# Optimization experiments

Measured on AMD Instinct MI355X. Metric: run time of the kernel, lower is better.

Reference implementation:

```python
import jax, jax.numpy as jnp
import numpy as np

N0, N1, B = 260000, 10240, 1024
E0, E1 = 256000, 10240
IN_C, HID, OUT_C = 602, 256, 41


def setup_inputs() -> dict:
    key = jax.random.key(0)
    ks = jax.random.split(key, 12)
    x = jax.random.normal(ks[0], (N0, IN_C), dtype=jnp.float32)
    W_l0 = jax.random.normal(ks[1], (IN_C, HID), dtype=jnp.float32) / np.sqrt(IN_C)
    b_l0 = jnp.zeros((HID,), dtype=jnp.float32)
    W_r0 = jax.random.normal(ks[2], (IN_C, HID), dtype=jnp.float32) / np.sqrt(IN_C)
    W_l1 = jax.random.normal(ks[3], (HID, OUT_C), dtype=jnp.float32) / np.sqrt(HID)
    b_l1 = jnp.zeros((OUT_C,), dtype=jnp.float32)
    W_r1 = jax.random.normal(ks[4], (HID, OUT_C), dtype=jnp.float32) / np.sqrt(HID)
    src0 = jax.random.randint(ks[5], (E0,), 0, N0)
    dst0 = jnp.sort(jax.random.randint(ks[6], (E0,), 0, N1))
    src1 = jax.random.randint(ks[7], (E1,), 0, N1)
    dst1 = jnp.sort(jax.random.randint(ks[8], (E1,), 0, B))
    return {"x": x, "W_l0": W_l0, "b_l0": b_l0, "W_r0": W_r0,
            "W_l1": W_l1, "b_l1": b_l1, "W_r1": W_r1,
            "src0": src0, "dst0": dst0, "src1": src1, "dst1": dst1}


def _sage_conv(x_src, x_tgt, src, dst, num_tgt, W_l, b_l, W_r):
    # mean aggregation of neighbor messages (PyG SAGEConv, mean aggr)
    msg = x_src[src]                                             # [E, C]
    s = jax.ops.segment_sum(msg, dst, num_segments=num_tgt)     # [Nt, C]
    cnt = jax.ops.segment_sum(jnp.ones((src.shape[0], 1), x_src.dtype),
                              dst, num_segments=num_tgt)         # [Nt, 1]
    agg = s / jnp.maximum(cnt, 1.0)
    # out = lin_l(agg) + lin_r(x_target); lin_r has no bias in PyG
    return agg @ W_l + b_l + x_tgt @ W_r


def reference(x, W_l0, b_l0, W_r0, W_l1, b_l1, W_r1, src0, dst0, src1, dst1):
    # layer 0: N0 sources -> N1 targets (targets are first N1 rows of x)
    h = _sage_conv(x, x[:N1], src0, dst0, N1, W_l0, b_l0, W_r0)
    h = jax.nn.relu(h)  # dropout is identity in eval mode
    # layer 1: N1 sources -> B targets
    out = _sage_conv(h, h[:B], src1, dst1, B, W_l1, b_l1, W_r1)
    return jax.nn.log_softmax(out, axis=-1)
```

## Files before the change

kernel.cpp:

```cpp
#include <hip/hip_runtime.h>
#include <math.h>

constexpr int cN0  = 260000;
constexpr int cN1  = 10240;
constexpr int cB   = 1024;
constexpr int cE0  = 256000;
constexpr int cE1  = 10240;
constexpr int cIN  = 602;
constexpr int cHID = 256;
constexpr int cOUT = 41;
constexpr int KP   = 608;

__device__ __forceinline__ int lower_bound_dev(const int* __restrict__ a, int n, int v) {
    int l = 0, r = n;
    while (l < r) { int m = (l + r) >> 1; if (a[m] < v) l = m + 1; else r = m; }
    return l;
}

__global__ __launch_bounds__(256) void k_agg0(
    const float* __restrict__ x, const int* __restrict__ src0,
    const int* __restrict__ dst0, float* __restrict__ agg0,
    float* __restrict__ xpad)
{
    const int t   = blockIdx.x;
    const int tid = threadIdx.x;
    const int lo  = lower_bound_dev(dst0, cE0, t);
    const int hi  = lower_bound_dev(dst0, cE0, t + 1);
    const int cnt = hi - lo;

    float a0 = 0.f, a1 = 0.f, a2 = 0.f;
    __shared__ int s_src[256];
    for (int base = lo; base < hi; base += 256) {
        const int n = min(256, hi - base);
        __syncthreads();
        if (tid < n) s_src[tid] = src0[base + tid];
        __syncthreads();
        for (int j = 0; j < n; ++j) {
            const float* row = x + (long)s_src[j] * cIN;
            a0 += row[tid];
            a1 += row[tid + 256];
            if (tid < cIN - 512) a2 += row[tid + 512];
        }
    }

    const float inv = 1.f / (float)(cnt > 1 ? cnt : 1);
    float*       og = agg0 + (long)t * KP;
    float*       ox = xpad + (long)t * KP;
    const float* xr = x    + (long)t * cIN;

    og[tid]       = a0 * inv;   ox[tid]       = xr[tid];
    og[tid + 256] = a1 * inv;   ox[tid + 256] = xr[tid + 256];
    if (tid < cIN - 512) {
        og[tid + 512] = a2 * inv;
        ox[tid + 512] = xr[tid + 512];
    } else if (tid < KP - 512) {
        og[tid + 512] = 0.f;
        ox[tid + 512] = 0.f;
    }
}

__global__ __launch_bounds__(256) void k_gemm1(
    const float* __restrict__ agg0, const float* __restrict__ xpad,
    const float* __restrict__ Wl,   const float* __restrict__ Wr,
    const float* __restrict__ bias, float* __restrict__ h)
{
    const int tid = threadIdx.x;
    const int n0  = (blockIdx.x & 3) * 64;
    const int m0  = (blockIdx.x >> 2) * 64;

    __shared__ float As[16][68];
    __shared__ float Bs[16][68];

    float acc[4][4] = {};
    const int tx = tid & 15, ty = tid >> 4;
    const int ai = tid >> 2, ak = (tid & 3) * 4;
    const int bk = tid >> 4, bj = (tid & 15) * 4;

    for (int phase = 0; phase < 2; ++phase) {
        const float* A = phase ? xpad : agg0;
        const float* W = phase ? Wr   : Wl;
        for (int k0 = 0; k0 < KP; k0 += 16) {
            __syncthreads();
            const float4 av = *(const float4*)(A + (long)(m0 + ai) * KP + k0 + ak);
            As[ak + 0][ai] = av.x;
            As[ak + 1][ai] = av.y;
            As[ak + 2][ai] = av.z;
            As[ak + 3][ai] = av.w;
            const int kg = k0 + bk;
            float4 bv = make_float4(0.f, 0.f, 0.f, 0.f);
            if (kg < cIN) bv = *(const float4*)(W + (long)kg * cHID + n0 + bj);
            Bs[bk][bj + 0] = bv.x;
            Bs[bk][bj + 1] = bv.y;
            Bs[bk][bj + 2] = bv.z;
            Bs[bk][bj + 3] = bv.w;
            __syncthreads();
            #pragma unroll
            for (int kk = 0; kk < 16; ++kk) {
                const float4 a4 = *(const float4*)&As[kk][ty * 4];
                const float4 b4 = *(const float4*)&Bs[kk][tx * 4];
                acc[0][0] += a4.x * b4.x; acc[0][1] += a4.x * b4.y;
                acc[0][2] += a4.x * b4.z; acc[0][3] += a4.x * b4.w;
                acc[1][0] += a4.y * b4.x; acc[1][1] += a4.y * b4.y;
                acc[1][2] += a4.y * b4.z; acc[1][3] += a4.y * b4.w;
                acc[2][0] += a4.z * b4.x; acc[2][1] += a4.z * b4.y;
                acc[2][2] += a4.z * b4.z; acc[2][3] += a4.z * b4.w;
                acc[3][0] += a4.w * b4.x; acc[3][1] += a4.w * b4.y;
                acc[3][2] += a4.w * b4.z; acc[3][3] += a4.w * b4.w;
            }
        }
    }

    #pragma unroll
    for (int i = 0; i < 4; ++i) {
        const int m = m0 + ty * 4 + i;
        float4 o;
        o.x = fmaxf(acc[i][0] + bias[n0 + tx * 4 + 0], 0.f);
        o.y = fmaxf(acc[i][1] + bias[n0 + tx * 4 + 1], 0.f);
        o.z = fmaxf(acc[i][2] + bias[n0 + tx * 4 + 2], 0.f);
        o.w = fmaxf(acc[i][3] + bias[n0 + tx * 4 + 3], 0.f);
        *(float4*)(h + (long)m * cHID + n0 + tx * 4) = o;
    }
}

__global__ __launch_bounds__(256) void k_agg1(
    const float* __restrict__ h, const int* __restrict__ src1,
    const int* __restrict__ dst1, float* __restrict__ agg1)
{
    const int t   = blockIdx.x;
    const int tid = threadIdx.x;
    const int lo  = lower_bound_dev(dst1, cE1, t);
    const int hi  = lower_bound_dev(dst1, cE1, t + 1);
    const int cnt = hi - lo;

    float a = 0.f;
    __shared__ int s_src[256];
    for (int base = lo; base < hi; base += 256) {
        const int n = min(256, hi - base);
        __syncthreads();
        if (tid < n) s_src[tid] = src1[base + tid];
        __syncthreads();
        for (int j = 0; j < n; ++j) a += h[(long)s_src[j] * cHID + tid];
    }
    agg1[(long)t * cHID + tid] = a / (float)(cnt > 1 ? cnt : 1);
}

__global__ __launch_bounds__(64) void k_out(
    const float* __restrict__ h,  const float* __restrict__ agg1,
    const float* __restrict__ Wl, const float* __restrict__ bias,
    const float* __restrict__ Wr, float* __restrict__ out)
{
    const int row = blockIdx.x;
    const int tid = threadIdx.x;
    __shared__ float sA[cHID], sH[cHID];
    for (int i = tid; i < cHID; i += 64) {
        sA[i] = agg1[(long)row * cHID + i];
        sH[i] = h[(long)row * cHID + i];
    }
    __syncthreads();

    float v = 0.f;
    if (tid < cOUT) {
        v = bias[tid];
        for (int k = 0; k < cHID; ++k)
            v += sA[k] * Wl[k * cOUT + tid] + sH[k] * Wr[k * cOUT + tid];
    }
    float lg = (tid < cOUT) ? v : -INFINITY;
    float m = lg;
    #pragma unroll
    for (int off = 32; off > 0; off >>= 1) m = fmaxf(m, __shfl_down(m, off));
    m = __shfl(m, 0);
    float e = (tid < cOUT) ? expf(v - m) : 0.f;
    float s = e;
    #pragma unroll
    for (int off = 32; off > 0; off >>= 1) s += __shfl_down(s, off);
    s = __shfl(s, 0);
    if (tid < cOUT) out[(long)row * cOUT + tid] = v - m - logf(s);
}

extern "C" void kernel_launch(void* const* d_in, const int* in_sizes, int n_in,
                              void* d_out, int out_size, void* d_ws, size_t ws_size,
                              hipStream_t stream)
{
    const float* x    = (const float*)d_in[0];
    const float* Wl0  = (const float*)d_in[1];
    const float* bl0  = (const float*)d_in[2];
    const float* Wr0  = (const float*)d_in[3];
    const float* Wl1  = (const float*)d_in[4];
    const float* bl1  = (const float*)d_in[5];
    const float* Wr1  = (const float*)d_in[6];
    const int*   src0 = (const int*)d_in[7];
    const int*   dst0 = (const int*)d_in[8];
    const int*   src1 = (const int*)d_in[9];
    const int*   dst1 = (const int*)d_in[10];
    float* out = (float*)d_out;

    char* ws = (char*)d_ws;
    const size_t szPad = (size_t)cN1 * KP * sizeof(float);
    float* agg0 = (float*)(ws);
    float* xpad = (float*)(ws + szPad);
    float* h    = (float*)(ws + 2 * szPad);
    float* agg1 = (float*)(ws + 2 * szPad + (size_t)cN1 * cHID * sizeof(float));

    k_agg0<<<cN1, 256, 0, stream>>>(x, src0, dst0, agg0, xpad);
    k_gemm1<<<(cN1 / 64) * 4, 256, 0, stream>>>(agg0, xpad, Wl0, Wr0, bl0, h);
    k_agg1<<<cB, 256, 0, stream>>>(h, src1, dst1, agg1);
    k_out<<<cB, 64, 0, stream>>>(h, agg1, Wl1, bl1, Wr1, out);
}
```

Baseline: 957.6 us.

## Use bf16 MFMA GEMM with concatenated [agg|x] operand and transposed bf16 weights

The aggregation kernel now writes one bf16 row holding the concatenated mean-aggregated features and the target features, instead of two fp32 padded buffers. A new pre-kernel transposes and concatenates W_l0 and W_r0 into a bf16 K-major matrix. The layer-0 GEMM becomes a single K=1216 pass using mfma_f32_16x16x32_bf16 instead of scalar fp32 FMA tiles, which cuts compute and memory traffic. The cost is bf16 rounding of activations and weights, an extra weight-prep launch on every call, and unvectorized scattered stores of h.

```diff
diff --git a/kernel.cpp b/kernel.cpp
--- a/kernel.cpp
+++ b/kernel.cpp
@@ -1,7 +1,7 @@
 #include <hip/hip_runtime.h>
+#include <hip/hip_bf16.h>
 #include <math.h>
 
-constexpr int cN0  = 260000;
 constexpr int cN1  = 10240;
 constexpr int cB   = 1024;
 constexpr int cE0  = 256000;
@@ -9,7 +9,10 @@
 constexpr int cIN  = 602;
 constexpr int cHID = 256;
 constexpr int cOUT = 41;
-constexpr int KP   = 608;
+constexpr int KC   = 1216;
+
+typedef __attribute__((ext_vector_type(8))) short short8;
+typedef __attribute__((ext_vector_type(4))) float f32x4;
 
 __device__ __forceinline__ int lower_bound_dev(const int* __restrict__ a, int n, int v) {
     int l = 0, r = n;
@@ -19,8 +22,7 @@
 
 __global__ __launch_bounds__(256) void k_agg0(
     const float* __restrict__ x, const int* __restrict__ src0,
-    const int* __restrict__ dst0, float* __restrict__ agg0,
-    float* __restrict__ xpad)
+    const int* __restrict__ dst0, __hip_bfloat16* __restrict__ cat)
 {
     const int t   = blockIdx.x;
     const int tid = threadIdx.x;
@@ -44,82 +46,89 @@
     }
 
     const float inv = 1.f / (float)(cnt > 1 ? cnt : 1);
-    float*       og = agg0 + (long)t * KP;
-    float*       ox = xpad + (long)t * KP;
-    const float* xr = x    + (long)t * cIN;
-
-    og[tid]       = a0 * inv;   ox[tid]       = xr[tid];
-    og[tid + 256] = a1 * inv;   ox[tid + 256] = xr[tid + 256];
-    if (tid < cIN - 512) {
-        og[tid + 512] = a2 * inv;
-        ox[tid + 512] = xr[tid + 512];
-    } else if (tid < KP - 512) {
-        og[tid + 512] = 0.f;
-        ox[tid + 512] = 0.f;
-    }
-}
-
-__global__ __launch_bounds__(256) void k_gemm1(
-    const float* __restrict__ agg0, const float* __restrict__ xpad,
-    const float* __restrict__ Wl,   const float* __restrict__ Wr,
+    __hip_bfloat16* cr = cat + (long)t * KC;
+    const float*    xr = x   + (long)t * cIN;
+
+    cr[tid]             = __float2bfloat16(a0 * inv);
+    cr[tid + 256]       = __float2bfloat16(a1 * inv);
+    cr[608 + tid]       = __float2bfloat16(xr[tid]);
+    cr[608 + 256 + tid] = __float2bfloat16(xr[tid + 256]);
+    if (tid < 96) {
+        const float va = (tid < 90) ? a2 * inv      : 0.f;
+        const float vx = (tid < 90) ? xr[512 + tid] : 0.f;
+        cr[512 + tid]       = __float2bfloat16(va);
+        cr[608 + 512 + tid] = __float2bfloat16(vx);
+    }
+}
+
+__global__ __launch_bounds__(256) void k_prep_w(
+    const float* __restrict__ Wl, const float* __restrict__ Wr,
+    __hip_bfloat16* __restrict__ Wt)
+{
+    const int idx = blockIdx.x * 256 + threadIdx.x;
+    const int n = idx / KC, k = idx - n * KC;
+    float v = 0.f;
+    if (k < cIN)                        v = Wl[(long)k * cHID + n];
+    else if (k >= 608 && k < 608 + cIN) v = Wr[(long)(k - 608) * cHID + n];
+    Wt[idx] = __float2bfloat16(v);
+}
+
+__global__ __launch_bounds__(256) void k_gemm(
+    const __hip_bfloat16* __restrict__ cat, const __hip_bfloat16* __restrict__ Wt,
     const float* __restrict__ bias, float* __restrict__ h)
 {
-    const int tid = threadIdx.x;
-    const int n0  = (blockIdx.x & 3) * 64;
-    const int m0  = (blockIdx.x >> 2) * 64;
-
-    __shared__ float As[16][68];
-    __shared__ float Bs[16][68];
-
-    float acc[4][4] = {};
-    const int tx = tid & 15, ty = tid >> 4;
-    const int ai = tid >> 2, ak = (tid & 3) * 4;
-    const int bk = tid >> 4, bj = (tid & 15) * 4;
-
-    for (int phase = 0; phase < 2; ++phase) {
-        const float* A = phase ? xpad : agg0;
-        const float* W = phase ? Wr   : Wl;
-        for (int k0 = 0; k0 < KP; k0 += 16) {
-            __syncthreads();
-            const float4 av = *(const float4*)(A + (long)(m0 + ai) * KP + k0 + ak);
-            As[ak + 0][ai] = av.x;
-            As[ak + 1][ai] = av.y;
-            As[ak + 2][ai] = av.z;
-            As[ak + 3][ai] = av.w;
-            const int kg = k0 + bk;
-            float4 bv = make_float4(0.f, 0.f, 0.f, 0.f);
-            if (kg < cIN) bv = *(const float4*)(W + (long)kg * cHID + n0 + bj);
-            Bs[bk][bj + 0] = bv.x;
-            Bs[bk][bj + 1] = bv.y;
-            Bs[bk][bj + 2] = bv.z;
-            Bs[bk][bj + 3] = bv.w;
-            __syncthreads();
+    const int tid  = threadIdx.x;
+    const int m0   = (blockIdx.x >> 2) * 64;
+    const int n0   = (blockIdx.x & 3) * 64;
+    const int w    = tid >> 6, lane = tid & 63;
+    const int wm   = (w & 1) * 32, wn = (w >> 1) * 32;
+    const int lrow = lane & 15, quad = lane >> 4;
+
+    __shared__ __hip_bfloat16 As[64 * 32];
+    __shared__ __hip_bfloat16 Bs[64 * 32];
+
+    f32x4 acc[2][2] = {};
+
+    const int srow = tid >> 2, schunk = tid & 3;
+    const __hip_bfloat16* gA = cat + (long)(m0 + srow) * KC + schunk * 8;
+    const __hip_bfloat16* gB = Wt  + (long)(n0 + srow) * KC + schunk * 8;
+    __hip_bfloat16* lA = As + srow * 32 + schunk * 8;
+    __hip_bfloat16* lB = Bs + srow * 32 + schunk * 8;
+
+    for (int k0 = 0; k0 < KC; k0 += 32) {
+        const short8 av = *(const short8*)(gA + k0);
+        const short8 bv = *(const short8*)(gB + k0);
+        __syncthreads();
+        *(short8*)lA = av;
+        *(short8*)lB = bv;
+        __syncthreads();
+
+        short8 af[2], bf[2];
+        #pragma unroll
+        for (int f = 0; f < 2; ++f) {
+            af[f] = *(const short8*)(As + (wm + f * 16 + lrow) * 32 + quad * 8);
+            bf[f] = *(const short8*)(Bs + (wn + f * 16 + lrow) * 32 + quad * 8);
+        }
+        #pragma unroll
+        for (int fm = 0; fm < 2; ++fm)
             #pragma unroll
-            for (int kk = 0; kk < 16; ++kk) {
-                const float4 a4 = *(const float4*)&As[kk][ty * 4];
-                const float4 b4 = *(const float4*)&Bs[kk][tx * 4];
-                acc[0][0] += a4.x * b4.x; acc[0][1] += a4.x * b4.y;
-                acc[0][2] += a4.x * b4.z; acc[0][3] += a4.x * b4.w;
-                acc[1][0] += a4.y * b4.x; acc[1][1] += a4.y * b4.y;
-                acc[1][2] += a4.y * b4.z; acc[1][3] += a4.y * b4.w;
-                acc[2][0] += a4.z * b4.x; acc[2][1] += a4.z * b4.y;
-                acc[2][2] += a4.z * b4.z; acc[2][3] += a4.z * b4.w;
-                acc[3][0] += a4.w * b4.x; acc[3][1] += a4.w * b4.y;
-                acc[3][2] += a4.w * b4.z; acc[3][3] += a4.w * b4.w;
+            for (int fn = 0; fn < 2; ++fn)
+                acc[fm][fn] = __builtin_amdgcn_mfma_f32_16x16x32_bf16(
+                    af[fm], bf[fn], acc[fm][fn], 0, 0, 0);
+    }
+
+    #pragma unroll
+    for (int fm = 0; fm < 2; ++fm)
+        #pragma unroll
+        for (int fn = 0; fn < 2; ++fn) {
+            const int col = n0 + wn + fn * 16 + lrow;
+            const float b = bias[col];
+            #pragma unroll
+            for (int r = 0; r < 4; ++r) {
+                const int row = m0 + wm + fm * 16 + quad * 4 + r;
+                h[(long)row * cHID + col] = fmaxf(acc[fm][fn][r] + b, 0.f);
             }
         }
-    }
-
-    #pragma unroll
-    for (int i = 0; i < 4; ++i) {
-        const int m = m0 + ty * 4 + i;
-        float4 o;
-        o.x = fmaxf(acc[i][0] + bias[n0 + tx * 4 + 0], 0.f);
-        o.y = fmaxf(acc[i][1] + bias[n0 + tx * 4 + 1], 0.f);
-        o.z = fmaxf(acc[i][2] + bias[n0 + tx * 4 + 2], 0.f);
-        o.w = fmaxf(acc[i][3] + bias[n0 + tx * 4 + 3], 0.f);
-        *(float4*)(h + (long)m * cHID + n0 + tx * 4) = o;
-    }
 }
 
 __global__ __launch_bounds__(256) void k_agg1(
@@ -195,14 +204,17 @@
     float* out = (float*)d_out;
 
     char* ws = (char*)d_ws;
-    const size_t szPad = (size_t)cN1 * KP * sizeof(float);
-    float* agg0 = (float*)(ws);
-    float* xpad = (float*)(ws + szPad);
-    float* h    = (float*)(ws + 2 * szPad);
-    float* agg1 = (float*)(ws + 2 * szPad + (size_t)cN1 * cHID * sizeof(float));
-
-    k_agg0<<<cN1, 256, 0, stream>>>(x, src0, dst0, agg0, xpad);
-    k_gemm1<<<(cN1 / 64) * 4, 256, 0, stream>>>(agg0, xpad, Wl0, Wr0, bl0, h);
+    const size_t szCat = (size_t)cN1 * KC * sizeof(__hip_bfloat16);
+    const size_t szWt  = (size_t)cHID * KC * sizeof(__hip_bfloat16);
+    const size_t szH   = (size_t)cN1 * cHID * sizeof(float);
+    __hip_bfloat16* cat  = (__hip_bfloat16*)(ws);
+    __hip_bfloat16* Wt   = (__hip_bfloat16*)(ws + szCat);
+    float*          h    = (float*)(ws + szCat + szWt);
+    float*          agg1 = (float*)(ws + szCat + szWt + szH);
+
+    k_prep_w<<<(cHID * KC) / 256, 256, 0, stream>>>(Wl0, Wr0, Wt);
+    k_agg0<<<cN1, 256, 0, stream>>>(x, src0, dst0, cat);
+    k_gemm<<<(cN1 / 64) * 4, 256, 0, stream>>>(cat, Wt, bl0, h);
     k_agg1<<<cB, 256, 0, stream>>>(h, src1, dst1, agg1);
     k_out<<<cB, 64, 0, stream>>>(h, agg1, Wl1, bl1, Wr1, out);
 }
```

Measured after the change: 871.0 us. 1.1x faster.
